# Kernel optimization log

Hardware: AMD Instinct MI355X
Metric: run time of the kernel (lower is better)

Reference implementation:

```python
import jax, jax.numpy as jnp
import numpy as np

BN_EPS = 1e-5


def _bn(y, g, b, m, v):
    # BatchNorm1d in eval mode (running stats), faithful to torch's affine BN
    return (y - m) * jax.lax.rsqrt(v + BN_EPS) * g + b


def setup_inputs() -> dict:
    key = jax.random.key(0)
    ks = jax.random.split(key, 6)
    N, E, C_IN, C_OUT = 20000, 640000, 128, 256
    x = jax.random.normal(ks[0], (N, C_IN), dtype=jnp.float32)
    tpl_edge_index = jax.random.randint(ks[1], (2, E), 0, N, dtype=jnp.int64)
    def lin(k, o, i):
        return jax.random.normal(k, (o, i), dtype=jnp.float32) * 0.05
    inp = {
        'x': x,
        'tpl_edge_index': tpl_edge_index,
        'W1': lin(ks[2], C_OUT, 2 * C_IN), 'b1': jnp.zeros((C_OUT,), jnp.float32),
        'g1': jnp.ones((C_OUT,), jnp.float32), 'be1': jnp.zeros((C_OUT,), jnp.float32),
        'm1': jnp.zeros((C_OUT,), jnp.float32), 'v1': jnp.ones((C_OUT,), jnp.float32),
        'W2': lin(ks[3], C_OUT, C_OUT), 'b2': jnp.zeros((C_OUT,), jnp.float32),
        'g2': jnp.ones((C_OUT,), jnp.float32), 'be2': jnp.zeros((C_OUT,), jnp.float32),
        'm2': jnp.zeros((C_OUT,), jnp.float32), 'v2': jnp.ones((C_OUT,), jnp.float32),
        'W3': lin(ks[4], C_OUT, C_OUT), 'b3': jnp.zeros((C_OUT,), jnp.float32),
        'g3': jnp.ones((C_OUT,), jnp.float32), 'be3': jnp.zeros((C_OUT,), jnp.float32),
        'm3': jnp.zeros((C_OUT,), jnp.float32), 'v3': jnp.ones((C_OUT,), jnp.float32),
    }
    return inp


def reference(x, tpl_edge_index, W1, b1, g1, be1, m1, v1,
              W2, b2, g2, be2, m2, v2, W3, b3, g3, be3, m3, v3):
    N = x.shape[0]
    # remove_self_loops + add_self_loops: under max aggregation, duplicate
    # self-loop messages (x_j - x_i == 0) are idempotent, so appending one
    # self-loop per node is mathematically identical.
    loops = jnp.arange(N, dtype=tpl_edge_index.dtype)
    src = jnp.concatenate([tpl_edge_index[0], loops])  # x_j indices
    tgt = jnp.concatenate([tpl_edge_index[1], loops])  # x_i / aggregation indices
    x_i = x[tgt]                                       # [E+N, C_in]
    x_j = x[src]
    h = jnp.concatenate([x_i, x_j - x_i], axis=1)      # [E+N, 2*C_in]
    h = _bn(jax.nn.relu(h @ W1.T + b1), g1, be1, m1, v1)
    h = _bn(jax.nn.relu(h @ W2.T + b2), g2, be2, m2, v2)
    agg = jax.ops.segment_max(h, tgt, num_segments=N)  # scatter-max -> [N, C_out]
    out = _bn(jax.nn.relu(agg @ W3.T + b3), g3, be3, m3, v3)
    return out
```

## Files before the change

### kernel.cpp

```cpp
#include <hip/hip_runtime.h>
#include <stdint.h>

#define BN_EPS 1e-5f

typedef __bf16 bf16x8 __attribute__((ext_vector_type(8)));
typedef __bf16 bf16x2 __attribute__((ext_vector_type(2)));
typedef float  f32x4  __attribute__((ext_vector_type(4)));
typedef float  f32x2  __attribute__((ext_vector_type(2)));

__device__ __forceinline__ unsigned short f2bf(float f) {
    unsigned u = __float_as_uint(f);
    unsigned r = (u + 0x7FFFu + ((u >> 16) & 1u)) >> 16;
    return (unsigned short)r;
}
__device__ __forceinline__ unsigned pkb(float a, float b) {
    f32x2 f; f.x = a; f.y = b;
    bf16x2 h = __builtin_convertvector(f, bf16x2);
    return *(unsigned*)&h;
}
__device__ __forceinline__ unsigned ar2(unsigned p, unsigned q) {
    f32x2 a, b;
    a.x = __uint_as_float(p << 16);
    a.y = __uint_as_float(p & 0xFFFF0000u);
    b.x = __uint_as_float(q << 16);
    b.y = __uint_as_float(q & 0xFFFF0000u);
    f32x2 s = a + b;
    return pkb(fmaxf(s.x, 0.f), fmaxf(s.y, 0.f));
}
__device__ __forceinline__ int swz(int row, int k) {
    const int blk = k >> 3;
    const int sb = (blk & 24) | ((blk ^ row) & 7);
    return (row << 8) + (sb << 3) + (k & 7);
}
__device__ __forceinline__ int swz128(int row, int k) {
    const int blk = k >> 3;
    const int sb = (blk & 8) | ((blk ^ row) & 7);
    return (row << 7) + (sb << 3) + (k & 7);
}

__global__ void prep_kernel(
    const float* __restrict__ x, const int* __restrict__ eidx,
    int E, int M, int NX,
    const float* __restrict__ W1, const float* __restrict__ W2, const float* __restrict__ W3,
    const float* __restrict__ b1, const float* __restrict__ g1, const float* __restrict__ be1,
    const float* __restrict__ m1, const float* __restrict__ v1,
    const float* __restrict__ b2, const float* __restrict__ g2, const float* __restrict__ be2,
    const float* __restrict__ m2, const float* __restrict__ v2,
    const float* __restrict__ b3, const float* __restrict__ g3, const float* __restrict__ be3,
    const float* __restrict__ m3, const float* __restrict__ v3,
    unsigned short* __restrict__ W1b, unsigned short* __restrict__ W2b,
    unsigned short* __restrict__ W3b, float* __restrict__ consts,
    unsigned* __restrict__ mask2,
    unsigned short* __restrict__ xb, unsigned* __restrict__ count)
{
    const int idx = blockIdx.x * 256 + threadIdx.x;
    if (idx < 65536) {
        const int row = idx >> 8, c = idx & 255;
        float w1v = (c < 128) ? (W1[row * 256 + c] - W1[row * 256 + c + 128])
                              : W1[row * 256 + c];
        W1b[idx] = f2bf(w1v);
        const float s1c = g1[c] * rsqrtf(v1[c] + BN_EPS);
        W2b[idx] = f2bf(W2[idx] * s1c);
        const float s2c = g2[c] * rsqrtf(v2[c] + BN_EPS);
        W3b[idx] = f2bf(W3[idx] * s2c);
    }
    if (idx < 128) {
        const float sa = g2[2 * idx]     * rsqrtf(v2[2 * idx]     + BN_EPS);
        const float sb = g2[2 * idx + 1] * rsqrtf(v2[2 * idx + 1] + BN_EPS);
        mask2[idx] = (sa < 0.f ? 0xFFFFu : 0u) | ((sb < 0.f ? 0xFFFFu : 0u) << 16);
    }
    if (idx < 768) {
        const int l = idx >> 8, c = idx & 255;
        const float* bp  = l == 0 ? b1  : (l == 1 ? b2  : b3);
        const float* gp  = l == 0 ? g1  : (l == 1 ? g2  : g3);
        const float* bep = l == 0 ? be1 : (l == 1 ? be2 : be3);
        const float* mp  = l == 0 ? m1  : (l == 1 ? m2  : m3);
        const float* vp  = l == 0 ? v1  : (l == 1 ? v2  : v3);
        const float s = gp[c] * rsqrtf(vp[c] + BN_EPS);
        float bias = bp[c];
        if (l == 1) {
            float acc = 0.f;
            for (int k = 0; k < 256; k++) {
                const float s1k = g1[k] * rsqrtf(v1[k] + BN_EPS);
                acc += W2[c * 256 + k] * (be1[k] - m1[k] * s1k);
            }
            bias += acc;
        } else if (l == 2) {
            float acc = 0.f;
            for (int k = 0; k < 256; k++) {
                const float s2k = g2[k] * rsqrtf(v2[k] + BN_EPS);
                acc += W3[c * 256 + k] * (be2[k] - m2[k] * s2k);
            }
            bias += acc;
        }
        consts[l * 768 + c]       = bias;
        consts[l * 768 + 256 + c] = s;
        consts[l * 768 + 512 + c] = bep[c] - mp[c] * s;
    }
    if (idx < NX) xb[idx] = f2bf(x[idx]);
    if (idx < M) {
        const int tgt = (idx < E) ? eidx[E + idx] : (idx - E);
        atomicAdd(&count[tgt], 1u);
    }
}

__global__ __launch_bounds__(512) void pq_kernel(
    const unsigned short* __restrict__ xb, int N,
    const unsigned short* __restrict__ W1b,
    const float* __restrict__ consts,
    unsigned short* __restrict__ Pb, unsigned short* __restrict__ Qb)
{
    __shared__ unsigned short Xs[64 * 128];

    const int t = threadIdx.x;
    const int base = blockIdx.x * 64;

    {
        const int row = t >> 3, part = t & 7;
        const int node = base + row;
        const int c0 = part * 16;
        if (node < N) {
            const unsigned short* s = xb + (size_t)node * 128 + c0;
            *(uint4*)&Xs[swz128(row, c0)]     = *(const uint4*)(s);
            *(uint4*)&Xs[swz128(row, c0 + 8)] = *(const uint4*)(s + 8);
        } else {
            const uint4 z = {0u, 0u, 0u, 0u};
            *(uint4*)&Xs[swz128(row, c0)]     = z;
            *(uint4*)&Xs[swz128(row, c0 + 8)] = z;
        }
    }
    __syncthreads();

    const int lane = t & 63;
    const int wv   = t >> 6;
    const int n16  = lane & 15;
    const int qd   = lane >> 4;
    const int wc   = wv * 32;

    const f32x4 vzero = {0.f, 0.f, 0.f, 0.f};

    #pragma unroll
    for (int ph = 0; ph < 2; ph++) {
        f32x4 acc[2][4];
        #pragma unroll
        for (int i = 0; i < 2; i++)
            #pragma unroll
            for (int j = 0; j < 4; j++) acc[i][j] = vzero;

        #pragma unroll
        for (int ks = 0; ks < 4; ks++) {
            const int k0 = ks * 32 + qd * 8;
            bf16x8 a[2], b[4];
            #pragma unroll
            for (int ci = 0; ci < 2; ci++)
                a[ci] = *(const bf16x8*)&W1b[(size_t)(wc + ci * 16 + n16) * 256 + ph * 128 + k0];
            #pragma unroll
            for (int rj = 0; rj < 4; rj++)
                b[rj] = *(const bf16x8*)&Xs[swz128(rj * 16 + n16, k0)];
            #pragma unroll
            for (int ci = 0; ci < 2; ci++)
                #pragma unroll
                for (int rj = 0; rj < 4; rj++)
                    acc[ci][rj] = __builtin_amdgcn_mfma_f32_16x16x32_bf16(a[ci], b[rj], acc[ci][rj], 0, 0, 0);
        }

        unsigned short* dst = ph == 0 ? Pb : Qb;
        #pragma unroll
        for (int ci = 0; ci < 2; ci++) {
            const int col0 = wc + ci * 16 + qd * 4;
            float4 bb = {0.f, 0.f, 0.f, 0.f};
            if (ph == 0) bb = *(const float4*)&consts[col0];
            #pragma unroll
            for (int rj = 0; rj < 4; rj++) {
                const int node = base + rj * 16 + n16;
                if (node < N) {
                    uint2 p = {pkb(acc[ci][rj][0] + bb.x, acc[ci][rj][1] + bb.y),
                               pkb(acc[ci][rj][2] + bb.z, acc[ci][rj][3] + bb.w)};
                    *(uint2*)(dst + (size_t)node * 256 + col0) = p;
                }
            }
        }
    }
}

__global__ __launch_bounds__(1024) void scan_kernel(
    const unsigned* __restrict__ count, unsigned* __restrict__ cursor, int N)
{
    __shared__ unsigned part[1024];
    const int t = threadIdx.x;
    const int per = (N + 1023) / 1024;
    const int b = t * per;
    unsigned s = 0;
    for (int i = 0; i < per; i++) if (b + i < N) s += count[b + i];
    part[t] = s;
    __syncthreads();
    for (int off = 1; off < 1024; off <<= 1) {
        unsigned v = (t >= off) ? part[t - off] : 0u;
        __syncthreads();
        part[t] += v;
        __syncthreads();
    }
    unsigned run = (t > 0) ? part[t - 1] : 0u;
    for (int i = 0; i < per; i++) {
        if (b + i < N) {
            unsigned c = count[b + i];
            cursor[b + i] = run;
            run += c;
        }
    }
}

__global__ void scatter_kernel(const int* __restrict__ eidx, int E, int M,
                               unsigned* __restrict__ cursor, int* __restrict__ spair)
{
    const int i = blockIdx.x * 256 + threadIdx.x;
    if (i < M) {
        int s, tg;
        if (i < E) { s = eidx[i]; tg = eidx[E + i]; }
        else       { s = tg = i - E; }
        const unsigned pos = atomicAdd(&cursor[tg], 1u);
        int2* p = (int2*)spair;
        p[pos] = make_int2(s, tg);
    }
}

__global__ __launch_bounds__(512) void msg_kernel(
    const unsigned short* __restrict__ Pb,
    const unsigned short* __restrict__ Qb,
    const int* __restrict__ spair,
    int M,
    const unsigned short* __restrict__ W2b,
    const float* __restrict__ consts,
    const unsigned* __restrict__ mask2,
    unsigned* __restrict__ agg)
{
    __shared__ unsigned short At[64 * 256];
    __shared__ int tgt_l[64];

    const int t = threadIdx.x;
    const int base = blockIdx.x * 64;

    {
        const int row = t >> 3, part = t & 7;
        const int slot = base + row;
        const int c0 = part * 32;
        if (slot < M) {
            const int2 pr = *(const int2*)(spair + 2 * slot);
            if (part == 0) tgt_l[row] = pr.y;
            const unsigned short* Pp = Pb + (size_t)pr.y * 256 + c0;
            const unsigned short* Qp = Qb + (size_t)pr.x * 256 + c0;
            uint4 P4[4], Q4[4];
            #pragma unroll
            for (int w = 0; w < 4; w++) P4[w] = *(const uint4*)(Pp + w * 8);
            #pragma unroll
            for (int w = 0; w < 4; w++) Q4[w] = *(const uint4*)(Qp + w * 8);
            #pragma unroll
            for (int w = 0; w < 4; w++) {
                uint4 u;
                u.x = ar2(P4[w].x, Q4[w].x);
                u.y = ar2(P4[w].y, Q4[w].y);
                u.z = ar2(P4[w].z, Q4[w].z);
                u.w = ar2(P4[w].w, Q4[w].w);
                *(uint4*)&At[swz(row, c0 + w * 8)] = u;
            }
        } else {
            if (part == 0) tgt_l[row] = -1;
            const uint4 z = {0u, 0u, 0u, 0u};
            #pragma unroll
            for (int w = 0; w < 4; w++) *(uint4*)&At[swz(row, c0 + w * 8)] = z;
        }
    }
    __syncthreads();

    const int lane = t & 63;
    const int wv   = t >> 6;
    const int n16  = lane & 15;
    const int qd   = lane >> 4;
    const int wc   = wv * 32;

    const f32x4 vzero = {0.f, 0.f, 0.f, 0.f};
    f32x4 acc[2][4];
    #pragma unroll
    for (int i = 0; i < 2; i++)
        #pragma unroll
        for (int j = 0; j < 4; j++) acc[i][j] = vzero;

    #pragma unroll
    for (int ks = 0; ks < 8; ks++) {
        const int k0 = ks * 32 + qd * 8;
        bf16x8 a[2], b[4];
        #pragma unroll
        for (int ci = 0; ci < 2; ci++)
            a[ci] = *(const bf16x8*)&W2b[(size_t)(wc + ci * 16 + n16) * 256 + k0];
        #pragma unroll
        for (int rj = 0; rj < 4; rj++)
            b[rj] = *(const bf16x8*)&At[swz(rj * 16 + n16, k0)];
        #pragma unroll
        for (int ci = 0; ci < 2; ci++)
            #pragma unroll
            for (int rj = 0; rj < 4; rj++)
                acc[ci][rj] = __builtin_amdgcn_mfma_f32_16x16x32_bf16(a[ci], b[rj], acc[ci][rj], 0, 0, 0);
    }
    __syncthreads();

    {
        const float* B2 = consts + 768;
        #pragma unroll
        for (int ci = 0; ci < 2; ci++) {
            const int col0 = wc + ci * 16 + qd * 4;
            const float4 bb = *(const float4*)&B2[col0];
            const uint2 mk = *(const uint2*)&mask2[col0 >> 1];
            #pragma unroll
            for (int rj = 0; rj < 4; rj++) {
                const int row = rj * 16 + n16;
                float r0 = fmaxf(acc[ci][rj][0] + bb.x, 0.f);
                float r1 = fmaxf(acc[ci][rj][1] + bb.y, 0.f);
                float r2 = fmaxf(acc[ci][rj][2] + bb.z, 0.f);
                float r3 = fmaxf(acc[ci][rj][3] + bb.w, 0.f);
                uint2 p = {pkb(r0, r1) ^ mk.x, pkb(r2, r3) ^ mk.y};
                *(uint2*)&At[swz(row, col0)] = p;
            }
        }
    }
    __syncthreads();

    {
        const int r0 = (wv & 3) * 16;
        const int cb = (wv >> 2) * 128 + lane * 2;
        const int myt = (lane < 16) ? tgt_l[r0 + lane] : -1;
        int curT = -1;
        unsigned m0 = 0, m1 = 0;
        for (int r = 0; r < 16; r++) {
            const int tg = __shfl(myt, r);
            const unsigned k2 = *(const unsigned*)&At[swz(r0 + r, cb)];
            const unsigned k0 = k2 & 0xFFFFu, k1 = k2 >> 16;
            if (tg != curT) {
                if (curT >= 0) {
                    unsigned* p = &agg[(size_t)curT * 256 + cb];
                    atomicMax(p, m0); atomicMax(p + 1, m1);
                }
                curT = tg; m0 = k0; m1 = k1;
            } else {
                m0 = m0 > k0 ? m0 : k0;
                m1 = m1 > k1 ? m1 : k1;
            }
        }
        if (curT >= 0) {
            unsigned* p = &agg[(size_t)curT * 256 + cb];
            atomicMax(p, m0); atomicMax(p + 1, m1);
        }
    }
}

__global__ __launch_bounds__(256) void out_kernel(
    const unsigned* __restrict__ agg, int N,
    const unsigned short* __restrict__ W3b,
    const float* __restrict__ consts,
    const unsigned* __restrict__ mask2,
    float* __restrict__ out)
{
    __shared__ unsigned short At[32 * 256];

    const int t = threadIdx.x;
    const int base = blockIdx.x * 32;

    {
        const int row = t >> 3, part = t & 7;
        const int node = base + row;
        const int c0 = part * 32;
        if (node < N) {
            const unsigned* ap = agg + (size_t)node * 256 + c0;
            #pragma unroll
            for (int w = 0; w < 4; w++) {
                uint4 a = *(const uint4*)(ap + w * 8);
                uint4 b = *(const uint4*)(ap + w * 8 + 4);
                const uint4 mk = *(const uint4*)&mask2[(c0 + w * 8) >> 1];
                uint4 p;
                p.x = (a.x | (a.y << 16)) ^ mk.x;
                p.y = (a.z | (a.w << 16)) ^ mk.y;
                p.z = (b.x | (b.y << 16)) ^ mk.z;
                p.w = (b.z | (b.w << 16)) ^ mk.w;
                *(uint4*)&At[swz(row, c0 + w * 8)] = p;
            }
        } else {
            const uint4 z = {0u, 0u, 0u, 0u};
            #pragma unroll
            for (int w = 0; w < 4; w++) *(uint4*)&At[swz(row, c0 + w * 8)] = z;
        }
    }
    __syncthreads();

    const int lane = t & 63;
    const int wv   = t >> 6;
    const int n16  = lane & 15;
    const int qd   = lane >> 4;
    const int wc   = wv * 64;

    const f32x4 vzero = {0.f, 0.f, 0.f, 0.f};
    f32x4 acc[2][4];
    #pragma unroll
    for (int i = 0; i < 2; i++)
        #pragma unroll
        for (int j = 0; j < 4; j++) acc[i][j] = vzero;

    #pragma unroll
    for (int ks = 0; ks < 8; ks++) {
        const int k0 = ks * 32 + qd * 8;
        bf16x8 a[2];
        #pragma unroll
        for (int ri = 0; ri < 2; ri++)
            a[ri] = *(const bf16x8*)&At[swz(ri * 16 + n16, k0)];
        #pragma unroll
        for (int ci = 0; ci < 4; ci++) {
            bf16x8 b = *(const bf16x8*)&W3b[(size_t)(wc + ci * 16 + n16) * 256 + k0];
            #pragma unroll
            for (int ri = 0; ri < 2; ri++)
                acc[ri][ci] = __builtin_amdgcn_mfma_f32_16x16x32_bf16(a[ri], b, acc[ri][ci], 0, 0, 0);
        }
    }

    {
        const float* B3 = consts + 1536;
        const float* S3 = consts + 1536 + 256;
        const float* T3 = consts + 1536 + 512;
        #pragma unroll
        for (int ci = 0; ci < 4; ci++) {
            const int col = wc + ci * 16 + n16;
            const float bb = B3[col], ss = S3[col], tt = T3[col];
            #pragma unroll
            for (int ri = 0; ri < 2; ri++) {
                #pragma unroll
                for (int r = 0; r < 4; r++) {
                    const int row = ri * 16 + qd * 4 + r;
                    const int node = base + row;
                    if (node < N) {
                        float v = fmaxf(acc[ri][ci][r] + bb, 0.f) * ss + tt;
                        out[(size_t)node * 256 + col] = v;
                    }
                }
            }
        }
    }
}

extern "C" void kernel_launch(void* const* d_in, const int* in_sizes, int n_in,
                              void* d_out, int out_size, void* d_ws, size_t ws_size,
                              hipStream_t stream)
{
    const float* x  = (const float*)d_in[0];
    const int* eidx = (const int*)d_in[1];
    const int N = in_sizes[0] / 128;
    const int NX = in_sizes[0];
    const int E = in_sizes[1] / 2;
    const int M = E + N;

    char* ws = (char*)d_ws;
    unsigned short* W1b = (unsigned short*)(ws);
    unsigned short* W2b = (unsigned short*)(ws + 131072);
    unsigned short* W3b = (unsigned short*)(ws + 262144);
    float* consts       = (float*)(ws + 393216);
    unsigned* mask2     = (unsigned*)(ws + 402432);
    size_t off = 402944;
    unsigned short* xb  = (unsigned short*)(ws + off); off += (size_t)NX * 2;
    unsigned* agg       = (unsigned*)(ws + off);       off += (size_t)N * 256 * 4;
    unsigned* count     = (unsigned*)(ws + off);       off += (size_t)N * 4;
    unsigned* cursor    = (unsigned*)(ws + off);       off += (size_t)N * 4;
    int* spair          = (int*)(ws + off);            off += (size_t)M * 8;
    unsigned short* Pb  = (unsigned short*)(ws + off); off += (size_t)N * 256 * 2;
    unsigned short* Qb  = (unsigned short*)(ws + off);

    hipMemsetAsync(agg, 0, (size_t)N * 256 * 4, stream);
    hipMemsetAsync(count, 0, (size_t)N * 4, stream);

    int work = NX;
    if (M > work) work = M;
    if (65536 > work) work = 65536;
    hipLaunchKernelGGL(prep_kernel, dim3((work + 255) / 256), dim3(256), 0, stream,
        x, eidx, E, M, NX,
        (const float*)d_in[2], (const float*)d_in[8], (const float*)d_in[14],
        (const float*)d_in[3], (const float*)d_in[4], (const float*)d_in[5],
        (const float*)d_in[6], (const float*)d_in[7],
        (const float*)d_in[9], (const float*)d_in[10], (const float*)d_in[11],
        (const float*)d_in[12], (const float*)d_in[13],
        (const float*)d_in[15], (const float*)d_in[16], (const float*)d_in[17],
        (const float*)d_in[18], (const float*)d_in[19],
        W1b, W2b, W3b, consts, mask2, xb, count);

    hipLaunchKernelGGL(pq_kernel, dim3((N + 63) / 64), dim3(512), 0, stream,
        xb, N, W1b, consts, Pb, Qb);

    hipLaunchKernelGGL(scan_kernel, dim3(1), dim3(1024), 0, stream,
        count, cursor, N);
    hipLaunchKernelGGL(scatter_kernel, dim3((M + 255) / 256), dim3(256), 0, stream,
        eidx, E, M, cursor, spair);

    hipLaunchKernelGGL(msg_kernel, dim3((M + 63) / 64), dim3(512), 0, stream,
        Pb, Qb, spair, M, W2b, consts, mask2, agg);

    hipLaunchKernelGGL(out_kernel, dim3((N + 31) / 32), dim3(256), 0, stream,
        agg, N, W3b, consts, mask2, (float*)d_out);
}
```

Before: 490.9 us.

## Pipeline msg kernel over multiple tiles, fuse x conversion, parallelize bias matvec

The message kernel now handles TPB tiles per block with a double-buffered shared tile, so the gathers for the next tile are issued while the current tile runs its MFMA, epilogue and scatter-max. The x-to-bf16 conversion moves into pq_kernel, dropping a separate workspace pass. The serial per-thread 256-length bias dot products in prep_kernel move to a warp-parallel matvec kernel, and the scan reads counts with vector loads. In exchange the message kernel uses twice the shared memory and more registers, and one extra kernel launch is added.

```diff
diff --git a/kernel.cpp b/kernel.cpp
--- a/kernel.cpp
+++ b/kernel.cpp
@@ -2,6 +2,7 @@
 #include <stdint.h>
 
 #define BN_EPS 1e-5f
+#define TPB 8
 
 typedef __bf16 bf16x8 __attribute__((ext_vector_type(8)));
 typedef __bf16 bf16x2 __attribute__((ext_vector_type(2)));
@@ -39,8 +40,8 @@
 }
 
 __global__ void prep_kernel(
-    const float* __restrict__ x, const int* __restrict__ eidx,
-    int E, int M, int NX,
+    const int* __restrict__ eidx,
+    int E, int M,
     const float* __restrict__ W1, const float* __restrict__ W2, const float* __restrict__ W3,
     const float* __restrict__ b1, const float* __restrict__ g1, const float* __restrict__ be1,
     const float* __restrict__ m1, const float* __restrict__ v1,
@@ -50,8 +51,7 @@
     const float* __restrict__ m3, const float* __restrict__ v3,
     unsigned short* __restrict__ W1b, unsigned short* __restrict__ W2b,
     unsigned short* __restrict__ W3b, float* __restrict__ consts,
-    unsigned* __restrict__ mask2,
-    unsigned short* __restrict__ xb, unsigned* __restrict__ count)
+    unsigned* __restrict__ mask2, unsigned* __restrict__ count)
 {
     const int idx = blockIdx.x * 256 + threadIdx.x;
     if (idx < 65536) {
@@ -77,35 +77,35 @@
         const float* mp  = l == 0 ? m1  : (l == 1 ? m2  : m3);
         const float* vp  = l == 0 ? v1  : (l == 1 ? v2  : v3);
         const float s = gp[c] * rsqrtf(vp[c] + BN_EPS);
-        float bias = bp[c];
-        if (l == 1) {
-            float acc = 0.f;
-            for (int k = 0; k < 256; k++) {
-                const float s1k = g1[k] * rsqrtf(v1[k] + BN_EPS);
-                acc += W2[c * 256 + k] * (be1[k] - m1[k] * s1k);
-            }
-            bias += acc;
-        } else if (l == 2) {
-            float acc = 0.f;
-            for (int k = 0; k < 256; k++) {
-                const float s2k = g2[k] * rsqrtf(v2[k] + BN_EPS);
-                acc += W3[c * 256 + k] * (be2[k] - m2[k] * s2k);
-            }
-            bias += acc;
-        }
-        consts[l * 768 + c]       = bias;
+        consts[l * 768 + c]       = bp[c];
         consts[l * 768 + 256 + c] = s;
         consts[l * 768 + 512 + c] = bep[c] - mp[c] * s;
     }
-    if (idx < NX) xb[idx] = f2bf(x[idx]);
     if (idx < M) {
         const int tgt = (idx < E) ? eidx[E + idx] : (idx - E);
         atomicAdd(&count[tgt], 1u);
     }
 }
 
+__global__ __launch_bounds__(256) void matvec_kernel(
+    const float* __restrict__ W2, const float* __restrict__ W3,
+    float* __restrict__ consts)
+{
+    const int g = blockIdx.x * 4 + (threadIdx.x >> 6);
+    const int lane = threadIdx.x & 63;
+    const int l = g >> 8, c = g & 255;
+    const float* W = l ? W3 : W2;
+    const float* tv = consts + (l ? (768 + 512) : 512);
+    float4 w4 = *(const float4*)&W[c * 256 + lane * 4];
+    float4 t4 = *(const float4*)&tv[lane * 4];
+    float s = w4.x * t4.x + w4.y * t4.y + w4.z * t4.z + w4.w * t4.w;
+    #pragma unroll
+    for (int d = 1; d < 64; d <<= 1) s += __shfl_xor(s, d);
+    if (lane == 0) consts[(l ? 1536 : 768) + c] += s;
+}
+
 __global__ __launch_bounds__(512) void pq_kernel(
-    const unsigned short* __restrict__ xb, int N,
+    const float* __restrict__ x, int N,
     const unsigned short* __restrict__ W1b,
     const float* __restrict__ consts,
     unsigned short* __restrict__ Pb, unsigned short* __restrict__ Qb)
@@ -120,9 +120,15 @@
         const int node = base + row;
         const int c0 = part * 16;
         if (node < N) {
-            const unsigned short* s = xb + (size_t)node * 128 + c0;
-            *(uint4*)&Xs[swz128(row, c0)]     = *(const uint4*)(s);
-            *(uint4*)&Xs[swz128(row, c0 + 8)] = *(const uint4*)(s + 8);
+            const float* s = x + (size_t)node * 128 + c0;
+            float4 a0 = *(const float4*)(s);
+            float4 a1 = *(const float4*)(s + 4);
+            float4 a2 = *(const float4*)(s + 8);
+            float4 a3 = *(const float4*)(s + 12);
+            uint4 p0 = {pkb(a0.x, a0.y), pkb(a0.z, a0.w), pkb(a1.x, a1.y), pkb(a1.z, a1.w)};
+            uint4 p1 = {pkb(a2.x, a2.y), pkb(a2.z, a2.w), pkb(a3.x, a3.y), pkb(a3.z, a3.w)};
+            *(uint4*)&Xs[swz128(row, c0)]     = p0;
+            *(uint4*)&Xs[swz128(row, c0 + 8)] = p1;
         } else {
             const uint4 z = {0u, 0u, 0u, 0u};
             *(uint4*)&Xs[swz128(row, c0)]     = z;
@@ -191,7 +197,14 @@
     const int per = (N + 1023) / 1024;
     const int b = t * per;
     unsigned s = 0;
-    for (int i = 0; i < per; i++) if (b + i < N) s += count[b + i];
+    if (b + per <= N && (per & 3) == 0) {
+        for (int i = 0; i < per; i += 4) {
+            uint4 c4 = *(const uint4*)(count + b + i);
+            s += c4.x + c4.y + c4.z + c4.w;
+        }
+    } else {
+        for (int i = 0; i < per; i++) if (b + i < N) s += count[b + i];
+    }
     part[t] = s;
     __syncthreads();
     for (int off = 1; off < 1024; off <<= 1) {
@@ -224,7 +237,7 @@
     }
 }
 
-__global__ __launch_bounds__(512) void msg_kernel(
+__global__ __launch_bounds__(512, 4) void msg_kernel(
     const unsigned short* __restrict__ Pb,
     const unsigned short* __restrict__ Qb,
     const int* __restrict__ spair,
@@ -234,77 +247,84 @@
     const unsigned* __restrict__ mask2,
     unsigned* __restrict__ agg)
 {
-    __shared__ unsigned short At[64 * 256];
-    __shared__ int tgt_l[64];
+    __shared__ unsigned short At[2][64 * 256];
 
     const int t = threadIdx.x;
-    const int base = blockIdx.x * 64;
-
-    {
-        const int row = t >> 3, part = t & 7;
-        const int slot = base + row;
-        const int c0 = part * 32;
-        if (slot < M) {
-            const int2 pr = *(const int2*)(spair + 2 * slot);
-            if (part == 0) tgt_l[row] = pr.y;
-            const unsigned short* Pp = Pb + (size_t)pr.y * 256 + c0;
-            const unsigned short* Qp = Qb + (size_t)pr.x * 256 + c0;
-            uint4 P4[4], Q4[4];
-            #pragma unroll
-            for (int w = 0; w < 4; w++) P4[w] = *(const uint4*)(Pp + w * 8);
-            #pragma unroll
-            for (int w = 0; w < 4; w++) Q4[w] = *(const uint4*)(Qp + w * 8);
-            #pragma unroll
-            for (int w = 0; w < 4; w++) {
-                uint4 u;
-                u.x = ar2(P4[w].x, Q4[w].x);
-                u.y = ar2(P4[w].y, Q4[w].y);
-                u.z = ar2(P4[w].z, Q4[w].z);
-                u.w = ar2(P4[w].w, Q4[w].w);
-                *(uint4*)&At[swz(row, c0 + w * 8)] = u;
-            }
-        } else {
-            if (part == 0) tgt_l[row] = -1;
-            const uint4 z = {0u, 0u, 0u, 0u};
-            #pragma unroll
-            for (int w = 0; w < 4; w++) *(uint4*)&At[swz(row, c0 + w * 8)] = z;
-        }
-    }
-    __syncthreads();
-
+    const int row = t >> 3, part = t & 7;
+    const int c0 = part * 32;
     const int lane = t & 63;
     const int wv   = t >> 6;
     const int n16  = lane & 15;
     const int qd   = lane >> 4;
     const int wc   = wv * 32;
+    const int tile0 = blockIdx.x * TPB;
+
+    uint4 P4[4], Q4[4];
+
+    auto loadTile = [&](int k) {
+        const int slot = (tile0 + k) * 64 + row;
+        if (slot < M) {
+            const int2 pr = *(const int2*)(spair + 2 * slot);
+            const unsigned short* Pp = Pb + (size_t)pr.y * 256 + c0;
+            const unsigned short* Qp = Qb + (size_t)pr.x * 256 + c0;
+            #pragma unroll
+            for (int w = 0; w < 4; w++) P4[w] = *(const uint4*)(Pp + w * 8);
+            #pragma unroll
+            for (int w = 0; w < 4; w++) Q4[w] = *(const uint4*)(Qp + w * 8);
+        } else {
+            const uint4 z = {0u, 0u, 0u, 0u};
+            #pragma unroll
+            for (int w = 0; w < 4; w++) { P4[w] = z; Q4[w] = z; }
+        }
+    };
+    auto writeU1 = [&](int buf) {
+        #pragma unroll
+        for (int w = 0; w < 4; w++) {
+            uint4 u;
+            u.x = ar2(P4[w].x, Q4[w].x);
+            u.y = ar2(P4[w].y, Q4[w].y);
+            u.z = ar2(P4[w].z, Q4[w].z);
+            u.w = ar2(P4[w].w, Q4[w].w);
+            *(uint4*)&At[buf][swz(row, c0 + w * 8)] = u;
+        }
+    };
+
+    loadTile(0);
+    writeU1(0);
+    __syncthreads();
 
     const f32x4 vzero = {0.f, 0.f, 0.f, 0.f};
-    f32x4 acc[2][4];
-    #pragma unroll
-    for (int i = 0; i < 2; i++)
-        #pragma unroll
-        for (int j = 0; j < 4; j++) acc[i][j] = vzero;
-
-    #pragma unroll
-    for (int ks = 0; ks < 8; ks++) {
-        const int k0 = ks * 32 + qd * 8;
-        bf16x8 a[2], b[4];
-        #pragma unroll
-        for (int ci = 0; ci < 2; ci++)
-            a[ci] = *(const bf16x8*)&W2b[(size_t)(wc + ci * 16 + n16) * 256 + k0];
-        #pragma unroll
-        for (int rj = 0; rj < 4; rj++)
-            b[rj] = *(const bf16x8*)&At[swz(rj * 16 + n16, k0)];
-        #pragma unroll
-        for (int ci = 0; ci < 2; ci++)
+    const float* B2 = consts + 768;
+
+    for (int i = 0; i < TPB; i++) {
+        const int u = i & 1, v = u ^ 1;
+
+        if (i + 1 < TPB) loadTile(i + 1);
+
+        f32x4 acc[2][4];
+        #pragma unroll
+        for (int a = 0; a < 2; a++)
+            #pragma unroll
+            for (int j = 0; j < 4; j++) acc[a][j] = vzero;
+
+        #pragma unroll
+        for (int ks = 0; ks < 8; ks++) {
+            const int k0 = ks * 32 + qd * 8;
+            bf16x8 a[2], b[4];
+            #pragma unroll
+            for (int ci = 0; ci < 2; ci++)
+                a[ci] = *(const bf16x8*)&W2b[(size_t)(wc + ci * 16 + n16) * 256 + k0];
             #pragma unroll
             for (int rj = 0; rj < 4; rj++)
-                acc[ci][rj] = __builtin_amdgcn_mfma_f32_16x16x32_bf16(a[ci], b[rj], acc[ci][rj], 0, 0, 0);
-    }
-    __syncthreads();
-
-    {
-        const float* B2 = consts + 768;
+                b[rj] = *(const bf16x8*)&At[u][swz(rj * 16 + n16, k0)];
+            #pragma unroll
+            for (int ci = 0; ci < 2; ci++)
+                #pragma unroll
+                for (int rj = 0; rj < 4; rj++)
+                    acc[ci][rj] = __builtin_amdgcn_mfma_f32_16x16x32_bf16(a[ci], b[rj], acc[ci][rj], 0, 0, 0);
+        }
+        __syncthreads();
+
         #pragma unroll
         for (int ci = 0; ci < 2; ci++) {
             const int col0 = wc + ci * 16 + qd * 4;
@@ -312,43 +332,46 @@
             const uint2 mk = *(const uint2*)&mask2[col0 >> 1];
             #pragma unroll
             for (int rj = 0; rj < 4; rj++) {
-                const int row = rj * 16 + n16;
+                const int rr = rj * 16 + n16;
                 float r0 = fmaxf(acc[ci][rj][0] + bb.x, 0.f);
                 float r1 = fmaxf(acc[ci][rj][1] + bb.y, 0.f);
                 float r2 = fmaxf(acc[ci][rj][2] + bb.z, 0.f);
                 float r3 = fmaxf(acc[ci][rj][3] + bb.w, 0.f);
                 uint2 p = {pkb(r0, r1) ^ mk.x, pkb(r2, r3) ^ mk.y};
-                *(uint2*)&At[swz(row, col0)] = p;
+                *(uint2*)&At[u][swz(rr, col0)] = p;
             }
         }
-    }
-    __syncthreads();
-
-    {
-        const int r0 = (wv & 3) * 16;
-        const int cb = (wv >> 2) * 128 + lane * 2;
-        const int myt = (lane < 16) ? tgt_l[r0 + lane] : -1;
-        int curT = -1;
-        unsigned m0 = 0, m1 = 0;
-        for (int r = 0; r < 16; r++) {
-            const int tg = __shfl(myt, r);
-            const unsigned k2 = *(const unsigned*)&At[swz(r0 + r, cb)];
-            const unsigned k0 = k2 & 0xFFFFu, k1 = k2 >> 16;
-            if (tg != curT) {
-                if (curT >= 0) {
-                    unsigned* p = &agg[(size_t)curT * 256 + cb];
-                    atomicMax(p, m0); atomicMax(p + 1, m1);
+        if (i + 1 < TPB) writeU1(v);
+        __syncthreads();
+
+        {
+            const int r0i = (wv & 3) * 16;
+            const int cb = (wv >> 2) * 128 + lane * 2;
+            const int slot = (tile0 + i) * 64 + r0i + lane;
+            const int myt = (lane < 16 && slot < M) ? spair[2 * slot + 1] : -1;
+            int curT = -1;
+            unsigned m0 = 0, m1 = 0;
+            for (int r = 0; r < 16; r++) {
+                const int tg = __shfl(myt, r);
+                const unsigned k2 = *(const unsigned*)&At[u][swz(r0i + r, cb)];
+                const unsigned k0 = k2 & 0xFFFFu, k1 = k2 >> 16;
+                if (tg != curT) {
+                    if (curT >= 0) {
+                        unsigned* p = &agg[(size_t)curT * 256 + cb];
+                        atomicMax(p, m0); atomicMax(p + 1, m1);
+                    }
+                    curT = tg; m0 = k0; m1 = k1;
+                } else {
+                    m0 = m0 > k0 ? m0 : k0;
+                    m1 = m1 > k1 ? m1 : k1;
                 }
-                curT = tg; m0 = k0; m1 = k1;
-            } else {
-                m0 = m0 > k0 ? m0 : k0;
-                m1 = m1 > k1 ? m1 : k1;
             }
-        }
-        if (curT >= 0) {
-            unsigned* p = &agg[(size_t)curT * 256 + cb];
-            atomicMax(p, m0); atomicMax(p + 1, m1);
-        }
+            if (curT >= 0) {
+                unsigned* p = &agg[(size_t)curT * 256 + cb];
+                atomicMax(p, m0); atomicMax(p + 1, m1);
+            }
+        }
+        __syncthreads();
     }
 }
 
@@ -450,9 +473,9 @@
     const float* x  = (const float*)d_in[0];
     const int* eidx = (const int*)d_in[1];
     const int N = in_sizes[0] / 128;
-    const int NX = in_sizes[0];
     const int E = in_sizes[1] / 2;
     const int M = E + N;
+    const int nTiles = (M + 63) / 64;
 
     char* ws = (char*)d_ws;
     unsigned short* W1b = (unsigned short*)(ws);
@@ -461,7 +484,6 @@
     float* consts       = (float*)(ws + 393216);
     unsigned* mask2     = (unsigned*)(ws + 402432);
     size_t off = 402944;
-    unsigned short* xb  = (unsigned short*)(ws + off); off += (size_t)NX * 2;
     unsigned* agg       = (unsigned*)(ws + off);       off += (size_t)N * 256 * 4;
     unsigned* count     = (unsigned*)(ws + off);       off += (size_t)N * 4;
     unsigned* cursor    = (unsigned*)(ws + off);       off += (size_t)N * 4;
@@ -472,11 +494,10 @@
     hipMemsetAsync(agg, 0, (size_t)N * 256 * 4, stream);
     hipMemsetAsync(count, 0, (size_t)N * 4, stream);
 
-    int work = NX;
-    if (M > work) work = M;
+    int work = M;
     if (65536 > work) work = 65536;
     hipLaunchKernelGGL(prep_kernel, dim3((work + 255) / 256), dim3(256), 0, stream,
-        x, eidx, E, M, NX,
+        eidx, E, M,
         (const float*)d_in[2], (const float*)d_in[8], (const float*)d_in[14],
         (const float*)d_in[3], (const float*)d_in[4], (const float*)d_in[5],
         (const float*)d_in[6], (const float*)d_in[7],
@@ -484,17 +505,20 @@
         (const float*)d_in[12], (const float*)d_in[13],
         (const float*)d_in[15], (const float*)d_in[16], (const float*)d_in[17],
         (const float*)d_in[18], (const float*)d_in[19],
-        W1b, W2b, W3b, consts, mask2, xb, count);
+        W1b, W2b, W3b, consts, mask2, count);
+
+    hipLaunchKernelGGL(matvec_kernel, dim3(128), dim3(256), 0, stream,
+        (const float*)d_in[8], (const float*)d_in[14], consts);
 
     hipLaunchKernelGGL(pq_kernel, dim3((N + 63) / 64), dim3(512), 0, stream,
-        xb, N, W1b, consts, Pb, Qb);
+        x, N, W1b, consts, Pb, Qb);
 
     hipLaunchKernelGGL(scan_kernel, dim3(1), dim3(1024), 0, stream,
         count, cursor, N);
     hipLaunchKernelGGL(scatter_kernel, dim3((M + 255) / 256), dim3(256), 0, stream,
         eidx, E, M, cursor, spair);
 
-    hipLaunchKernelGGL(msg_kernel, dim3((M + 63) / 64), dim3(512), 0, stream,
+    hipLaunchKernelGGL(msg_kernel, dim3((nTiles + TPB - 1) / TPB), dim3(512), 0, stream,
         Pb, Qb, spair, M, W2b, consts, mask2, agg);
 
     hipLaunchKernelGGL(out_kernel, dim3((N + 31) / 32), dim3(256), 0, stream,
```

Result: slower. 675.4 us (+37.6%).
